# Kernel tuning notes

Measured on AMD Instinct MI355X. Metric: run time of the kernel, lower is better.

## Reference

```python
import jax, jax.numpy as jnp
import numpy as np

B, N, DIM, H = 8, 1024, 768, 12
D = DIM // H  # head_dim = 64
SCALE = D ** -0.5


def setup_inputs() -> dict:
    key = jax.random.key(0)
    k1, k2, k3, k4 = jax.random.split(key, 4)
    x = jax.random.normal(k1, (B, N, DIM), dtype=jnp.float32)
    # nn.Linear(dim, dim*3, bias=False): weight [3*dim, dim]; y = x @ W^T
    w_qkv = jax.random.normal(k2, (3 * DIM, DIM), dtype=jnp.float32) * (DIM ** -0.5)
    # nn.Linear(dim, dim) with bias
    w_proj = jax.random.normal(k3, (DIM, DIM), dtype=jnp.float32) * (DIM ** -0.5)
    b_proj = jax.random.normal(k4, (DIM,), dtype=jnp.float32) * 0.01
    return {"x": x, "w_qkv": w_qkv, "w_proj": w_proj, "b_proj": b_proj}


def reference(x, w_qkv, w_proj, b_proj):
    b, n, dim = x.shape
    qkv = x @ w_qkv.T  # [b, n, 3*dim]
    # rearrange 'b n (h d qkv) -> qkv b h n d' (qkv innermost in the split)
    qkv = qkv.reshape(b, n, H, D, 3)
    qkv = jnp.transpose(qkv, (4, 0, 2, 1, 3))  # [3, b, h, n, d]
    q, k, v = qkv[0], qkv[1], qkv[2]
    energy = jnp.einsum('bhqd,bhkd->bhqk', q, k) * SCALE
    att = jax.nn.softmax(energy, axis=-1)  # dropout p=0.0 -> identity
    out = jnp.einsum('bhal,bhlv->bhav', att, v)  # [b, h, n, d]
    out = jnp.transpose(out, (0, 2, 1, 3)).reshape(b, n, dim)
    return out @ w_proj.T + b_proj
```

## Files before the change

### kernel.cpp

```cpp
#include <hip/hip_runtime.h>
#include <hip/hip_bf16.h>
#include <stdint.h>

#define NH 12

typedef __attribute__((ext_vector_type(8))) short bf16x8;
typedef __attribute__((ext_vector_type(4))) float f32x4;

static __device__ __forceinline__ ushort f2bf(float f) {
  union { float f; uint32_t u; } v; v.f = f;
  uint32_t r = (v.u + 0x7FFFu + ((v.u >> 16) & 1u)) >> 16;
  return (ushort)r;
}

static __device__ __forceinline__ uint32_t cvtpk(float lo, float hi) {
  uint32_t r;
  asm("v_cvt_pk_bf16_f32 %0, %1, %2" : "=v"(r) : "v"(lo), "v"(hi));
  return r;
}

static __device__ __forceinline__ void gl_lds16(const void* g, void* l) {
  __builtin_amdgcn_global_load_lds(
      (const __attribute__((address_space(1))) uint32_t*)(uintptr_t)g,
      (__attribute__((address_space(3))) uint32_t*)(uintptr_t)l,
      16, 0, 0);
}

static __device__ __forceinline__ f32x4 mfma32(bf16x8 a, bf16x8 b, f32x4 c) {
  return __builtin_amdgcn_mfma_f32_16x16x32_bf16(a, b, c, 0, 0, 0);
}

#define QSCALE 0.1803368801111601f

__global__ __launch_bounds__(256) void k_cvt(const float4* __restrict__ src,
                                             ushort4* __restrict__ dst, int n4) {
  int i = blockIdx.x * blockDim.x + threadIdx.x;
  if (i < n4) {
    float4 v = src[i];
    ushort4 o;
    o.x = f2bf(v.x); o.y = f2bf(v.y); o.z = f2bf(v.z); o.w = f2bf(v.w);
    dst[i] = o;
  }
}

__global__ __launch_bounds__(256) void k_cvt_wq(const float4* __restrict__ src,
                                                ushort4* __restrict__ dst) {
  int i = blockIdx.x * 256 + threadIdx.x;
  if (i >= 2304 * 192) return;
  int ro = i / 192, cc = i - ro * 192;
  int h = ro / 192;
  int rem = ro - h * 192;
  int d = rem / 3;
  int which = rem - d * 3;
  int rn = which * 768 + h * 64 + d;
  float4 v = src[i];
  ushort4 o;
  o.x = f2bf(v.x); o.y = f2bf(v.y); o.z = f2bf(v.z); o.w = f2bf(v.w);
  dst[(size_t)rn * 192 + cc] = o;
}

#define DECL_GEMM_VARS() \
  const int tid = threadIdx.x; \
  const int w = tid >> 6, l = tid & 63, g = l >> 4, c15 = l & 15; \
  const int wm = w >> 1, wn = w & 1; \
  const int dst0 = w * 1024 + l * 16; \
  const int row_s = w * 16 + (l >> 2); \
  const int cg = ((l & 3) ^ ((l >> 3) & 3)) * 8; \
  const int gsw = (g ^ ((c15 >> 1) & 3)) * 8;

#define STAGE(pa, pb, Aptr, Bptr, kk0) do { \
    gl_lds16((Aptr) + (size_t)(m0 + row_s) * 768 + (kk0) + cg, (char*)(pa) + dst0); \
    gl_lds16((Aptr) + (size_t)(m0 + row_s + 64) * 768 + (kk0) + cg, (char*)(pa) + dst0 + 4096); \
    gl_lds16((Bptr) + (size_t)(n0 + row_s) * 768 + (kk0) + cg, (char*)(pb) + dst0); \
    gl_lds16((Bptr) + (size_t)(n0 + row_s + 64) * 768 + (kk0) + cg, (char*)(pb) + dst0 + 4096); \
  } while (0)

#define COMPUTE(pa, pb) do { \
    bf16x8 af[4], bfr[4]; \
    _Pragma("unroll") \
    for (int i = 0; i < 4; i++) { \
      af[i]  = *(const bf16x8*)&(pa)[(wm * 64 + i * 16 + c15) * 32 + gsw]; \
      bfr[i] = *(const bf16x8*)&(pb)[(wn * 64 + i * 16 + c15) * 32 + gsw]; \
    } \
    _Pragma("unroll") \
    for (int mr = 0; mr < 4; mr++) \
      _Pragma("unroll") \
      for (int nr = 0; nr < 4; nr++) \
        acc[mr][nr] = mfma32(af[mr], bfr[nr], acc[mr][nr]); \
  } while (0)

__global__ __launch_bounds__(256, 4) void k_qkv(const ushort* __restrict__ X,
                                                const ushort* __restrict__ W,
                                                ushort* __restrict__ Qb,
                                                ushort* __restrict__ Kf,
                                                ushort* __restrict__ Vf) {
  __shared__ __align__(16) ushort lds[16384];
  const int id = (int)blockIdx.x;
  const int swz = (id & 7) * 144 + (id >> 3);
  const int bx = swz % 18, by = swz / 18;
  const int m0 = by * 128, n0 = bx * 128;
  DECL_GEMM_VARS();

  ushort* A0 = lds;
  ushort* A1 = lds + 4096;
  ushort* B0 = lds + 8192;
  ushort* B1 = lds + 12288;

  f32x4 acc[4][4] = {};

  STAGE(A0, B0, X, W, 0);
  __syncthreads();
#pragma unroll 1
  for (int k0 = 0; k0 < 768; k0 += 64) {
    STAGE(A1, B1, X, W, k0 + 32);
    COMPUTE(A0, B0);
    __syncthreads();
    if (k0 + 64 < 768) STAGE(A0, B0, X, W, k0 + 64);
    COMPUTE(A1, B1);
    __syncthreads();
  }

  const int type = bx / 6;
  const int cb = (bx % 6) * 128;
  const int h0 = cb >> 6;
  const int b = m0 >> 10, nbase = m0 & 1023, tbase = nbase >> 5;

  if (type == 0) {
#pragma unroll
    for (int nr = 0; nr < 4; nr++) {
      const int colrel = wn * 64 + nr * 16 + c15;
#pragma unroll
      for (int mr = 0; mr < 4; mr++)
#pragma unroll
        for (int r = 0; r < 4; r++) {
          const int mrel = wm * 64 + mr * 16 + 4 * g + r;
          lds[mrel * 128 + colrel] = f2bf(acc[mr][nr][r] * QSCALE);
        }
    }
    __syncthreads();
#pragma unroll
    for (int j = 0; j < 8; j++) {
      const int cid = j * 256 + tid;
      const int n = cid >> 4, coloff = (cid & 15) * 8;
      const int hrel = coloff >> 6, d0q = coloff & 63;
      bf16x8 vv = *(const bf16x8*)&lds[n * 128 + coloff];
      *(bf16x8*)(Qb + ((size_t)(b * NH + h0 + hrel) * 1024 + nbase + n) * 64 + d0q) = vv;
    }
  } else if (type == 1) {
#pragma unroll
    for (int nr = 0; nr < 4; nr++) {
      const int colrel = wn * 64 + nr * 16 + c15;
      const int hrel = colrel >> 6, d = colrel & 63;
      const int gk = (d >> 3) & 3, ek = d & 7, hi = d >> 5;
#pragma unroll
      for (int mr = 0; mr < 4; mr++)
#pragma unroll
        for (int r = 0; r < 4; r++) {
          const int mrel = wm * 64 + mr * 16 + 4 * g + r;
          const int trel = mrel >> 5, kk = mrel & 31;
          const int x = kk >> 3, s = (kk >> 2) & 1, y = kk & 3;
          lds[(hrel * 4 + trel) * 2048 + (2 * s + hi) * 512 +
              (gk * 16 + x * 4 + y) * 8 + ek] = f2bf(acc[mr][nr][r]);
        }
    }
    __syncthreads();
    const int c = tid >> 5, jj = tid & 31;
    ushort* dst = Kf + ((size_t)(b * NH + h0 + (c >> 2)) * 32 + tbase + (c & 3)) * 2048;
    const ushort* srcl = lds + c * 2048;
#pragma unroll
    for (int k2 = 0; k2 < 8; k2++)
      *(bf16x8*)(dst + jj * 8 + k2 * 256) = *(const bf16x8*)(srcl + jj * 8 + k2 * 256);
  } else {
#pragma unroll
    for (int nr = 0; nr < 4; nr++) {
      const int colrel = wn * 64 + nr * 16 + c15;
      const int hrel = colrel >> 6, d = colrel & 63;
      const int dtv = d >> 4, cv = d & 15;
#pragma unroll
      for (int mr = 0; mr < 4; mr++)
#pragma unroll
        for (int r = 0; r < 4; r++) {
          const int mrel = wm * 64 + mr * 16 + 4 * g + r;
          const int trel = mrel >> 5, kk = mrel & 31;
          const int gv = kk >> 3, ev = kk & 7;
          lds[(hrel * 4 + trel) * 2048 + dtv * 512 +
              (gv * 16 + cv) * 8 + ev] = f2bf(acc[mr][nr][r]);
        }
    }
    __syncthreads();
    const int c = tid >> 5, jj = tid & 31;
    ushort* dst = Vf + ((size_t)(b * NH + h0 + (c >> 2)) * 32 + tbase + (c & 3)) * 2048;
    const ushort* srcl = lds + c * 2048;
#pragma unroll
    for (int k2 = 0; k2 < 8; k2++)
      *(bf16x8*)(dst + jj * 8 + k2 * 256) = *(const bf16x8*)(srcl + jj * 8 + k2 * 256);
  }
}

__global__ __launch_bounds__(256, 3) void k_attn(const ushort* __restrict__ Qb,
                                                 const ushort* __restrict__ Kf,
                                                 const ushort* __restrict__ Vf,
                                                 ushort* __restrict__ Ab) {
  const int bh = blockIdx.x;
  const int tid = threadIdx.x;
  const int w = tid >> 6, l = tid & 63, g = l >> 4, c15 = l & 15;
  const int q0 = blockIdx.y * 128 + w * 32;

  bf16x8 qf0a, qf0b, qf1a, qf1b;
  {
    const ushort* qp = Qb + ((size_t)bh * 1024 + q0 + c15) * 64 + g * 8;
    qf0a = *(const bf16x8*)qp;
    qf0b = *(const bf16x8*)(qp + 32);
    qf1a = *(const bf16x8*)(qp + 1024);
    qf1b = *(const bf16x8*)(qp + 1024 + 32);
  }
  const ushort* kfb = Kf + (size_t)bh * 32 * 2048 + l * 8;
  const ushort* vfb = Vf + (size_t)bh * 32 * 2048 + l * 8;

  bf16x8 vones;
#pragma unroll
  for (int j = 0; j < 8; j++) vones[j] = (short)0x3F80;

  f32x4 o0[4] = {}, o1[4] = {};
  f32x4 ol0 = {}, ol1 = {};

  for (int t = 0; t < 32; t++) {
    const ushort* kp = kfb + t * 2048;
    bf16x8 ka0a = *(const bf16x8*)(kp);
    bf16x8 ka0b = *(const bf16x8*)(kp + 512);
    bf16x8 ka1a = *(const bf16x8*)(kp + 1024);
    bf16x8 ka1b = *(const bf16x8*)(kp + 1536);
    f32x4 s00 = {0.f,0.f,0.f,0.f}, s01 = {0.f,0.f,0.f,0.f};
    f32x4 s10 = {0.f,0.f,0.f,0.f}, s11 = {0.f,0.f,0.f,0.f};
    s00 = mfma32(ka0a, qf0a, s00); s00 = mfma32(ka0b, qf0b, s00);
    s01 = mfma32(ka0a, qf1a, s01); s01 = mfma32(ka0b, qf1b, s01);
    s10 = mfma32(ka1a, qf0a, s10); s10 = mfma32(ka1b, qf0b, s10);
    s11 = mfma32(ka1a, qf1a, s11); s11 = mfma32(ka1b, qf1b, s11);

    float p0[8], p1[8];
#pragma unroll
    for (int r = 0; r < 4; r++) {
      p0[r]     = exp2f(s00[r]);
      p0[4 + r] = exp2f(s10[r]);
      p1[r]     = exp2f(s01[r]);
      p1[4 + r] = exp2f(s11[r]);
    }

    union { uint32_t u[4]; bf16x8 v; } pa0, pa1;
#pragma unroll
    for (int j = 0; j < 4; j++) {
      pa0.u[j] = cvtpk(p0[2 * j], p0[2 * j + 1]);
      pa1.u[j] = cvtpk(p1[2 * j], p1[2 * j + 1]);
    }

    ol0 = mfma32(pa0.v, vones, ol0);
    ol1 = mfma32(pa1.v, vones, ol1);

    const ushort* vp = vfb + t * 2048;
#pragma unroll
    for (int dt = 0; dt < 4; dt++) {
      bf16x8 vb = *(const bf16x8*)(vp + dt * 512);
      o0[dt] = mfma32(pa0.v, vb, o0[dt]);
      o1[dt] = mfma32(pa1.v, vb, o1[dt]);
    }
  }

  float il0[4], il1[4];
#pragma unroll
  for (int r = 0; r < 4; r++) {
    il0[r] = __builtin_amdgcn_rcpf(ol0[r]);
    il1[r] = __builtin_amdgcn_rcpf(ol1[r]);
  }
  const int b = bh / NH, h = bh % NH;
#pragma unroll
  for (int dt = 0; dt < 4; dt++)
#pragma unroll
    for (int r = 0; r < 4; r++) {
      const int n = q0 + 4 * g + r;
      Ab[(size_t)(b * 1024 + n) * 768 + h * 64 + dt * 16 + c15] =
          f2bf(o0[dt][r] * il0[r]);
      Ab[(size_t)(b * 1024 + n + 16) * 768 + h * 64 + dt * 16 + c15] =
          f2bf(o1[dt][r] * il1[r]);
    }
}

__global__ __launch_bounds__(256, 4) void k_proj(const ushort* __restrict__ Ain,
                                                 const ushort* __restrict__ W,
                                                 const float* __restrict__ Bp,
                                                 float* __restrict__ Out) {
  __shared__ __align__(16) ushort lds[16384];
  const int id = (int)blockIdx.x;
  const int swz = (id & 7) * 48 + (id >> 3);
  const int bx = swz % 6, by = swz / 6;
  const int m0 = by * 128, n0 = bx * 128;
  DECL_GEMM_VARS();

  ushort* A0 = lds;
  ushort* A1 = lds + 4096;
  ushort* B0 = lds + 8192;
  ushort* B1 = lds + 12288;

  f32x4 acc[4][4] = {};

  STAGE(A0, B0, Ain, W, 0);
  __syncthreads();
#pragma unroll 1
  for (int k0 = 0; k0 < 768; k0 += 64) {
    STAGE(A1, B1, Ain, W, k0 + 32);
    COMPUTE(A0, B0);
    __syncthreads();
    if (k0 + 64 < 768) STAGE(A0, B0, Ain, W, k0 + 64);
    COMPUTE(A1, B1);
    __syncthreads();
  }

#pragma unroll
  for (int nr = 0; nr < 4; nr++) {
    const int cc = n0 + wn * 64 + nr * 16 + c15;
    const float bias = Bp[cc];
#pragma unroll
    for (int mr = 0; mr < 4; mr++) {
      const int mb = m0 + wm * 64 + mr * 16 + 4 * g;
#pragma unroll
      for (int r = 0; r < 4; r++) {
        const int m = mb + r;
        Out[(size_t)m * 768 + cc] = acc[mr][nr][r] + bias;
      }
    }
  }
}

extern "C" void kernel_launch(void* const* d_in, const int* in_sizes, int n_in,
                              void* d_out, int out_size, void* d_ws, size_t ws_size,
                              hipStream_t stream) {
  const float* X  = (const float*)d_in[0];
  const float* Wq = (const float*)d_in[1];
  const float* Wp = (const float*)d_in[2];
  const float* Bp = (const float*)d_in[3];
  float* Out = (float*)d_out;

  char* ws = (char*)d_ws;
  const size_t SZ = (size_t)96 * 1024 * 64 * sizeof(ushort);
  ushort* Qb  = (ushort*)(ws);
  ushort* Kf  = (ushort*)(ws + SZ);
  ushort* Vf  = (ushort*)(ws + 2 * SZ);
  ushort* Ab  = (ushort*)(ws + 3 * SZ);
  ushort* Xb  = (ushort*)(ws + 4 * SZ);
  ushort* Wqb = (ushort*)(ws + 5 * SZ);
  ushort* Wpb = (ushort*)(ws + 5 * SZ + 2304 * 768 * 2);

  const int nX = 8192 * 768 / 4, nWp = 768 * 768 / 4;
  k_cvt<<<(nX + 255) / 256, 256, 0, stream>>>((const float4*)X, (ushort4*)Xb, nX);
  k_cvt_wq<<<(2304 * 192 + 255) / 256, 256, 0, stream>>>((const float4*)Wq, (ushort4*)Wqb);
  k_cvt<<<(nWp + 255) / 256, 256, 0, stream>>>((const float4*)Wp, (ushort4*)Wpb, nWp);

  k_qkv<<<1152, 256, 0, stream>>>(Xb, Wqb, Qb, Kf, Vf);
  k_attn<<<dim3(96, 8), 256, 0, stream>>>(Qb, Kf, Vf, Ab);
  k_proj<<<384, 256, 0, stream>>>(Ab, Wpb, Bp, Out);
}
```

Before: 116.6 us.

## Triple-buffer GEMM LDS pipeline with partial vmcnt waits; prioritize MFMA in attention

Both GEMM kernels move from a double-buffered LDS scheme with full __syncthreads to a three-stage ring. Explicit s_waitcnt vmcnt(4) plus barrier lets one stage of global-to-LDS loads stay in flight while the previous stage is computed. This raises LDS per block to 48KB and lowers the launch-bounds occupancy hint from 4 to 3. The attention loop is unrolled by 2 and its MFMA sections are wrapped in s_setprio to favour matrix issue across waves.

```diff
diff --git a/kernel.cpp b/kernel.cpp
--- a/kernel.cpp
+++ b/kernel.cpp
@@ -89,12 +89,37 @@
         acc[mr][nr] = mfma32(af[mr], bfr[nr], acc[mr][nr]); \
   } while (0)
 
-__global__ __launch_bounds__(256, 4) void k_qkv(const ushort* __restrict__ X,
+#define WB4 do { __builtin_amdgcn_sched_barrier(0); \
+    asm volatile("s_waitcnt vmcnt(4)\n\ts_barrier" ::: "memory"); \
+    __builtin_amdgcn_sched_barrier(0); } while (0)
+#define WB0 do { __builtin_amdgcn_sched_barrier(0); \
+    asm volatile("s_waitcnt vmcnt(0)\n\ts_barrier" ::: "memory"); \
+    __builtin_amdgcn_sched_barrier(0); } while (0)
+#define PFENCE do { asm volatile("" ::: "memory"); \
+    __builtin_amdgcn_sched_barrier(0); } while (0)
+
+#define GEMM_PIPE(Aptr, Bptr) do { \
+    STAGE(A0, B0, Aptr, Bptr, 0); \
+    PFENCE; \
+    STAGE(A1, B1, Aptr, Bptr, 32); \
+    WB4; \
+    _Pragma("unroll 1") \
+    for (int k0 = 0; k0 < 672; k0 += 96) { \
+      STAGE(A2, B2, Aptr, Bptr, k0 + 64);  COMPUTE(A0, B0); WB4; \
+      STAGE(A0, B0, Aptr, Bptr, k0 + 96);  COMPUTE(A1, B1); WB4; \
+      STAGE(A1, B1, Aptr, Bptr, k0 + 128); COMPUTE(A2, B2); WB4; \
+    } \
+    STAGE(A2, B2, Aptr, Bptr, 736); COMPUTE(A0, B0); WB4; \
+    COMPUTE(A1, B1); WB0; \
+    COMPUTE(A2, B2); \
+  } while (0)
+
+__global__ __launch_bounds__(256, 3) void k_qkv(const ushort* __restrict__ X,
                                                 const ushort* __restrict__ W,
                                                 ushort* __restrict__ Qb,
                                                 ushort* __restrict__ Kf,
                                                 ushort* __restrict__ Vf) {
-  __shared__ __align__(16) ushort lds[16384];
+  __shared__ __align__(16) ushort lds[24576];
   const int id = (int)blockIdx.x;
   const int swz = (id & 7) * 144 + (id >> 3);
   const int bx = swz % 18, by = swz / 18;
@@ -103,22 +128,14 @@
 
   ushort* A0 = lds;
   ushort* A1 = lds + 4096;
-  ushort* B0 = lds + 8192;
-  ushort* B1 = lds + 12288;
+  ushort* A2 = lds + 8192;
+  ushort* B0 = lds + 12288;
+  ushort* B1 = lds + 16384;
+  ushort* B2 = lds + 20480;
 
   f32x4 acc[4][4] = {};
-
-  STAGE(A0, B0, X, W, 0);
+  GEMM_PIPE(X, W);
   __syncthreads();
-#pragma unroll 1
-  for (int k0 = 0; k0 < 768; k0 += 64) {
-    STAGE(A1, B1, X, W, k0 + 32);
-    COMPUTE(A0, B0);
-    __syncthreads();
-    if (k0 + 64 < 768) STAGE(A0, B0, X, W, k0 + 64);
-    COMPUTE(A1, B1);
-    __syncthreads();
-  }
 
   const int type = bx / 6;
   const int cb = (bx % 6) * 128;
@@ -224,6 +241,7 @@
   f32x4 o0[4] = {}, o1[4] = {};
   f32x4 ol0 = {}, ol1 = {};
 
+#pragma unroll 2
   for (int t = 0; t < 32; t++) {
     const ushort* kp = kfb + t * 2048;
     bf16x8 ka0a = *(const bf16x8*)(kp);
@@ -232,10 +250,12 @@
     bf16x8 ka1b = *(const bf16x8*)(kp + 1536);
     f32x4 s00 = {0.f,0.f,0.f,0.f}, s01 = {0.f,0.f,0.f,0.f};
     f32x4 s10 = {0.f,0.f,0.f,0.f}, s11 = {0.f,0.f,0.f,0.f};
+    __builtin_amdgcn_s_setprio(1);
     s00 = mfma32(ka0a, qf0a, s00); s00 = mfma32(ka0b, qf0b, s00);
     s01 = mfma32(ka0a, qf1a, s01); s01 = mfma32(ka0b, qf1b, s01);
     s10 = mfma32(ka1a, qf0a, s10); s10 = mfma32(ka1b, qf0b, s10);
     s11 = mfma32(ka1a, qf1a, s11); s11 = mfma32(ka1b, qf1b, s11);
+    __builtin_amdgcn_s_setprio(0);
 
     float p0[8], p1[8];
 #pragma unroll
@@ -253,16 +273,17 @@
       pa1.u[j] = cvtpk(p1[2 * j], p1[2 * j + 1]);
     }
 
+    const ushort* vp = vfb + t * 2048;
+    __builtin_amdgcn_s_setprio(1);
     ol0 = mfma32(pa0.v, vones, ol0);
     ol1 = mfma32(pa1.v, vones, ol1);
-
-    const ushort* vp = vfb + t * 2048;
 #pragma unroll
     for (int dt = 0; dt < 4; dt++) {
       bf16x8 vb = *(const bf16x8*)(vp + dt * 512);
       o0[dt] = mfma32(pa0.v, vb, o0[dt]);
       o1[dt] = mfma32(pa1.v, vb, o1[dt]);
     }
+    __builtin_amdgcn_s_setprio(0);
   }
 
   float il0[4], il1[4];
@@ -284,11 +305,11 @@
     }
 }
 
-__global__ __launch_bounds__(256, 4) void k_proj(const ushort* __restrict__ Ain,
+__global__ __launch_bounds__(256, 3) void k_proj(const ushort* __restrict__ Ain,
                                                  const ushort* __restrict__ W,
                                                  const float* __restrict__ Bp,
                                                  float* __restrict__ Out) {
-  __shared__ __align__(16) ushort lds[16384];
+  __shared__ __align__(16) ushort lds[24576];
   const int id = (int)blockIdx.x;
   const int swz = (id & 7) * 48 + (id >> 3);
   const int bx = swz % 6, by = swz / 6;
@@ -297,22 +318,13 @@
 
   ushort* A0 = lds;
   ushort* A1 = lds + 4096;
-  ushort* B0 = lds + 8192;
-  ushort* B1 = lds + 12288;
+  ushort* A2 = lds + 8192;
+  ushort* B0 = lds + 12288;
+  ushort* B1 = lds + 16384;
+  ushort* B2 = lds + 20480;
 
   f32x4 acc[4][4] = {};
-
-  STAGE(A0, B0, Ain, W, 0);
-  __syncthreads();
-#pragma unroll 1
-  for (int k0 = 0; k0 < 768; k0 += 64) {
-    STAGE(A1, B1, Ain, W, k0 + 32);
-    COMPUTE(A0, B0);
-    __syncthreads();
-    if (k0 + 64 < 768) STAGE(A0, B0, Ain, W, k0 + 64);
-    COMPUTE(A1, B1);
-    __syncthreads();
-  }
+  GEMM_PIPE(Ain, W);
 
 #pragma unroll
   for (int nr = 0; nr < 4; nr++) {
```

Result: slower. 120.6 us (+3.4%).
